# Optimization experiments

Measured on AMD Instinct MI355X. Metric: run time of the kernel, lower is better.

## Reference

```python
import jax, jax.numpy as jnp
import numpy as np

N_VALUES = 4
N_DIGITS = 7
N_CLASSES = 10
INPUT_DIM = 2048
BATCH = 32768


def setup_inputs() -> dict:
    key = jax.random.key(0)
    k1, k2, k3, k4 = jax.random.split(key, 4)
    hidden = jax.random.normal(k1, (BATCH, INPUT_DIM), dtype=jnp.float32)
    labels = jax.random.randint(k2, (BATCH, N_VALUES, N_DIGITS), 0, N_CLASSES, dtype=jnp.int64)
    H = N_VALUES * N_DIGITS  # 28 heads
    # nn.Linear default init: U(-1/sqrt(fan_in), 1/sqrt(fan_in))
    bound = 1.0 / np.sqrt(INPUT_DIM)
    W = jax.random.uniform(k3, (H, N_CLASSES, INPUT_DIM), minval=-bound, maxval=bound, dtype=jnp.float32)
    b = jax.random.uniform(k4, (H, N_CLASSES), minval=-bound, maxval=bound, dtype=jnp.float32)
    return {"hidden": hidden, "labels": labels, "W": W, "b": b}


def reference(hidden, labels, W, b):
    B = hidden.shape[0]
    # Fuse all 28 tiny GEMMs into one: [B,D] x [H,C,D] -> [B,H,C]
    logits = jnp.einsum('bd,hcd->bhc', hidden, W) + b  # [B, 28, 10]
    logits = logits.reshape(B, N_VALUES, N_DIGITS, N_CLASSES)
    # per-head cross entropy (mean over batch), summed over heads, / (n_values*n_digits)
    logp = jax.nn.log_softmax(logits, axis=-1)  # [B, V, D, C]
    nll = -jnp.take_along_axis(logp, labels[..., None], axis=-1)[..., 0]  # [B, V, D]
    loss = jnp.mean(nll, axis=0).sum() / (N_VALUES * N_DIGITS)
    return loss, logits
```

## Files before the change

kernel.cpp:

```cpp
#include <hip/hip_runtime.h>
#include <hip/hip_bf16.h>

#define BATCH   32768
#define DIM     2048
#define NHEADS  28
#define NCOLS   280
#define LOSS_SCALE (1.0f / (float)(BATCH * NHEADS))

typedef __attribute__((ext_vector_type(8))) short short8;
typedef __attribute__((ext_vector_type(4))) short s4vec;
typedef __attribute__((ext_vector_type(4))) float f32x4;

__device__ __forceinline__ short f2bf(float f) {
    union { __hip_bfloat16 h; short s; } u; u.h = __float2bfloat16(f); return u.s;
}

__global__ void mvh_swz(const float* __restrict__ W, short* __restrict__ Wswz) {
    int t = blockIdx.x * 256 + threadIdx.x;
    int lane = t & 63;
    int ks = (t >> 6) & 63;
    int nt = t >> 12;
    int n = nt * 16 + (lane & 15);
    int d = ks * 32 + (lane >> 4) * 8;
    short8 v;
    #pragma unroll
    for (int j = 0; j < 8; j++) v[j] = 0;
    if (n < NCOLS) {
        const float* src = W + (size_t)n * DIM + d;
        #pragma unroll
        for (int j = 0; j < 8; j++) v[j] = f2bf(src[j]);
    }
    *(short8*)(Wswz + (size_t)t * 8) = v;
}

#define BO(k)  (8192 + ((k) % 3) * 18432)
#define CL_PITCH 292

#define SB0() __builtin_amdgcn_sched_barrier(0)
#define BARV() do { SB0(); \
    if (wave < 2) { asm volatile("s_waitcnt vmcnt(4) lgkmcnt(0)" ::: "memory"); } \
    else          { asm volatile("s_waitcnt vmcnt(3) lgkmcnt(0)" ::: "memory"); } \
    __builtin_amdgcn_s_barrier(); SB0(); \
} while (0)
#define BAR0() do { SB0(); asm volatile("s_waitcnt vmcnt(0) lgkmcnt(0)" ::: "memory"); \
    __builtin_amdgcn_s_barrier(); SB0(); } while (0)

__global__ __launch_bounds__(512, 4)
void mvh_gemm(const float* __restrict__ hidden, const short* __restrict__ Wswz,
              const float* __restrict__ bias, float* __restrict__ logits,
              const int* __restrict__ labels, float* __restrict__ loss_out) {
    __shared__ __align__(16) char lds[63488];

    const int tid  = threadIdx.x;
    const int lane = tid & 63;
    const int wave = tid >> 6;
    const int kph   = wave >> 2;
    const int wsub  = (wave >> 1) & 1;
    const int nhalf = wave & 1;
    const int l15 = lane & 15, lhi = lane >> 4;
    const int rowbase = blockIdx.x * 64;

    const int ar  = tid >> 3;
    const int ak4 = (tid & 7) * 4;
    const float* gA1 = hidden + (size_t)(rowbase + ar) * DIM + ak4;
    const int awbyte = (ar >> 4) * 1024 + ((ar & 15) + 16 * (ak4 >> 3)) * 16 + (ak4 & 4) * 2;

    f32x4 acc0[9], acc1[9];
    #pragma unroll
    for (int n = 0; n < 9; n++) { acc0[n] = (f32x4)0.0f; acc1[n] = (f32x4)0.0f; }

    f32x4 gx, gy;

#define LOADA1(reg, t) do { reg = *(const f32x4*)(gA1 + (t) * 32); SB0(); } while (0)

#define WRITEA1(aoff, reg) do { \
    s4vec w_; \
    w_[0] = f2bf(reg[0]); w_[1] = f2bf(reg[1]); w_[2] = f2bf(reg[2]); w_[3] = f2bf(reg[3]); \
    *(s4vec*)(lds + (aoff) + awbyte) = w_; \
} while (0)

#define STAGE_B(boff, kt) do { \
    _Pragma("unroll") \
    for (int i_ = 0; i_ < 3; i_++) { \
        if (i_ < 2 || tid < 128) { \
            int g_ = (i_ < 2) ? (i_ * 512 + tid) : (1024 + tid); \
            const short* gp_ = Wswz + (size_t)((g_ >> 6) * 64 + (kt)) * 512 + (g_ & 63) * 8; \
            __builtin_amdgcn_global_load_lds((const __attribute__((address_space(1))) void*)gp_, \
                (__attribute__((address_space(3))) void*)(lds + (boff) + g_ * 16), 16, 0, 0); \
        } \
    } \
    SB0(); \
} while (0)

#define COMPUTE(aoff, boff) do { \
    short8 af0_ = *(const short8*)(lds + (aoff) + (wsub * 2 + 0) * 1024 + lane * 16); \
    short8 af1_ = *(const short8*)(lds + (aoff) + (wsub * 2 + 1) * 1024 + lane * 16); \
    _Pragma("unroll") \
    for (int n_ = 0; n_ < 9; n_++) { \
        short8 bf_ = *(const short8*)(lds + (boff) + (nhalf * 9 + n_) * 1024 + lane * 16); \
        acc0[n_] = __builtin_amdgcn_mfma_f32_16x16x32_bf16(af0_, bf_, acc0[n_], 0, 0, 0); \
        acc1[n_] = __builtin_amdgcn_mfma_f32_16x16x32_bf16(af1_, bf_, acc1[n_], 0, 0, 0); \
    } \
} while (0)

    LOADA1(gx, 0);
    STAGE_B(BO(0), 0);
    WRITEA1(0, gx);
    LOADA1(gy, 1);
    STAGE_B(BO(1), 1);
    BARV();

    #pragma unroll 1
    for (int tp = 0; tp < 32; tp++) {
        const int t = tp * 2;
        if (tp < 31) { LOADA1(gx, t + 2); STAGE_B(BO(t + 2), t + 2); }
        if (kph == 0) COMPUTE(0, BO(t));
        SB0();
        WRITEA1(4096, gy);
        if (tp < 31) { BARV(); } else { BAR0(); }
        if (tp < 31) { LOADA1(gy, t + 3); STAGE_B(BO(t + 3), t + 3); }
        if (kph == 1) COMPUTE(4096, BO(t + 1));
        SB0();
        if (tp < 31) WRITEA1(0, gx);
        if (tp < 31) { BARV(); } else { BAR0(); }
    }

#undef LOADA1
#undef WRITEA1
#undef STAGE_B
#undef COMPUTE

    float* Cl  = (float*)lds;
    float* red = (float*)(lds + 38912);
    float lsum = 0.0f;

    #pragma unroll 1
    for (int s = 0; s < 2; s++) {
        __syncthreads();
        if (kph == 1 && wsub == s) {
            #pragma unroll
            for (int nf = 0; nf < 9; nf++) {
                int c = nhalf * 144 + nf * 16 + l15;
                #pragma unroll
                for (int r = 0; r < 4; r++) {
                    Cl[(lhi * 4 + r) * CL_PITCH + c]      = acc0[nf][r];
                    Cl[(16 + lhi * 4 + r) * CL_PITCH + c] = acc1[nf][r];
                }
            }
        }
        __syncthreads();
        if (kph == 0 && wsub == s) {
            #pragma unroll
            for (int nf = 0; nf < 9; nf++) {
                int c = nhalf * 144 + nf * 16 + l15;
                #pragma unroll
                for (int r = 0; r < 4; r++) {
                    Cl[(lhi * 4 + r) * CL_PITCH + c]      += acc0[nf][r];
                    Cl[(16 + lhi * 4 + r) * CL_PITCH + c] += acc1[nf][r];
                }
            }
        }
        __syncthreads();
        #pragma unroll 1
        for (int i = tid; i < 32 * 70; i += 512) {
            int lr = i / 70, ch = i - lr * 70;
            f32x4 v  = *(const f32x4*)(Cl + lr * CL_PITCH + ch * 4);
            f32x4 bv = *(const f32x4*)(bias + ch * 4);
            *(f32x4*)(logits + (size_t)(rowbase + s * 32 + lr) * NCOLS + ch * 4) = v + bv;
        }
        #pragma unroll 1
        for (int p = tid; p < 32 * NHEADS; p += 512) {
            int lr = p / NHEADS, h = p - lr * NHEADS;
            const float* x  = Cl + lr * CL_PITCH + h * 10;
            const float* bb = bias + h * 10;
            float xv[10];
            #pragma unroll
            for (int j = 0; j < 10; j++) xv[j] = x[j] + bb[j];
            float mx = xv[0];
            #pragma unroll
            for (int j = 1; j < 10; j++) mx = fmaxf(mx, xv[j]);
            float sm = 0.0f;
            #pragma unroll
            for (int j = 0; j < 10; j++) sm += __expf(xv[j] - mx);
            int lab = labels[(size_t)(rowbase + s * 32 + lr) * NHEADS + h];
            float xl = xv[0];
            #pragma unroll
            for (int j = 1; j < 10; j++) xl = (lab == j) ? xv[j] : xl;
            lsum += mx + __logf(sm) - xl;
        }
    }

    #pragma unroll
    for (int off = 32; off > 0; off >>= 1)
        lsum += __shfl_down(lsum, off, 64);
    if (lane == 0) red[wave] = lsum;
    __syncthreads();
    if (tid == 0) {
        float t = red[0] + red[1] + red[2] + red[3]
                + red[4] + red[5] + red[6] + red[7];
        atomicAdd(loss_out, t * LOSS_SCALE);
    }
}

extern "C" void kernel_launch(void* const* d_in, const int* in_sizes, int n_in,
                              void* d_out, int out_size, void* d_ws, size_t ws_size,
                              hipStream_t stream) {
    const float* hidden = (const float*)d_in[0];
    const int* labels   = (const int*)d_in[1];
    const float* W      = (const float*)d_in[2];
    const float* bias   = (const float*)d_in[3];
    float* out = (float*)d_out;
    short* Wswz = (short*)d_ws;

    (void)hipMemsetAsync(d_out, 0, sizeof(float), stream);
    mvh_swz<<<288, 256, 0, stream>>>(W, Wswz);
    mvh_gemm<<<512, 512, 0, stream>>>(hidden, Wswz, bias, out + 1, labels, out);
}
```

Measured before the change: 104.3 us.

## Split GEMM N dimension across block pairs with 4-stage A/B pipeline

Each block now covers 64 rows and only half of the 280 output columns (140, padded to 144). Launching 1024 blocks instead of 512 raises parallelism, and each wave does 9 MFMAs per k-step instead of 18. The weight swizzle is re-laid out per half and per k-tile. The K loop now uses 4-slot A and B ring buffers, with two k-tiles issued per iteration, fewer barriers, and s_setprio around the MFMAs. The cost is that each hidden row is read from global memory twice, once by each block of the pair, though paired blocks are adjacent in launch order to share cache.

```diff
diff --git a/kernel.cpp b/kernel.cpp
--- a/kernel.cpp
+++ b/kernel.cpp
@@ -17,15 +17,19 @@
 
 __global__ void mvh_swz(const float* __restrict__ W, short* __restrict__ Wswz) {
     int t = blockIdx.x * 256 + threadIdx.x;
-    int lane = t & 63;
-    int ks = (t >> 6) & 63;
-    int nt = t >> 12;
-    int n = nt * 16 + (lane & 15);
-    int d = ks * 32 + (lane >> 4) * 8;
+    int kt = t / 1152;
+    int r  = t - kt * 1152;
+    int f  = r >> 6;
+    int l  = r & 63;
+    int nh2 = (f >= 9) ? 1 : 0;
+    int nf  = f - nh2 * 9;
+    int lc  = nf * 16 + (l & 15);
+    int n   = nh2 * 140 + lc;
+    int d   = kt * 32 + (l >> 4) * 8;
     short8 v;
     #pragma unroll
     for (int j = 0; j < 8; j++) v[j] = 0;
-    if (n < NCOLS) {
+    if (lc < 140) {
         const float* src = W + (size_t)n * DIM + d;
         #pragma unroll
         for (int j = 0; j < 8; j++) v[j] = f2bf(src[j]);
@@ -33,45 +37,45 @@
     *(short8*)(Wswz + (size_t)t * 8) = v;
 }
 
-#define BO(k)  (8192 + ((k) % 3) * 18432)
-#define CL_PITCH 292
+#define ASL(t) (((t) & 3) * 4096)
+#define BSL(t) (16384 + ((t) & 3) * 9216)
+#define CLP 148
 
 #define SB0() __builtin_amdgcn_sched_barrier(0)
-#define BARV() do { SB0(); \
-    if (wave < 2) { asm volatile("s_waitcnt vmcnt(4) lgkmcnt(0)" ::: "memory"); } \
-    else          { asm volatile("s_waitcnt vmcnt(3) lgkmcnt(0)" ::: "memory"); } \
-    __builtin_amdgcn_s_barrier(); SB0(); \
-} while (0)
-#define BAR0() do { SB0(); asm volatile("s_waitcnt vmcnt(0) lgkmcnt(0)" ::: "memory"); \
+#define BARV2() do { SB0(); asm volatile("s_waitcnt vmcnt(2) lgkmcnt(0)" ::: "memory"); \
+    __builtin_amdgcn_s_barrier(); SB0(); } while (0)
+#define BARV0() do { SB0(); asm volatile("s_waitcnt vmcnt(0) lgkmcnt(0)" ::: "memory"); \
     __builtin_amdgcn_s_barrier(); SB0(); } while (0)
 
 __global__ __launch_bounds__(512, 4)
 void mvh_gemm(const float* __restrict__ hidden, const short* __restrict__ Wswz,
               const float* __restrict__ bias, float* __restrict__ logits,
               const int* __restrict__ labels, float* __restrict__ loss_out) {
-    __shared__ __align__(16) char lds[63488];
+    __shared__ __align__(16) char lds[53248];
 
     const int tid  = threadIdx.x;
     const int lane = tid & 63;
     const int wave = tid >> 6;
-    const int kph   = wave >> 2;
-    const int wsub  = (wave >> 1) & 1;
-    const int nhalf = wave & 1;
+    const int kph  = wave >> 2;
+    const int wsub = wave & 3;
     const int l15 = lane & 15, lhi = lane >> 4;
-    const int rowbase = blockIdx.x * 64;
+    const int bid = blockIdx.x;
+    const int rowblk = ((bid >> 4) << 3) | (bid & 7);
+    const int nh2 = (bid >> 3) & 1;
+    const int rowbase = rowblk * 64;
 
     const int ar  = tid >> 3;
     const int ak4 = (tid & 7) * 4;
-    const float* gA1 = hidden + (size_t)(rowbase + ar) * DIM + ak4;
+    const float* gAbase = hidden + (size_t)(rowbase + ar) * DIM + ak4;
     const int awbyte = (ar >> 4) * 1024 + ((ar & 15) + 16 * (ak4 >> 3)) * 16 + (ak4 & 4) * 2;
 
-    f32x4 acc0[9], acc1[9];
+    f32x4 acc[9];
     #pragma unroll
-    for (int n = 0; n < 9; n++) { acc0[n] = (f32x4)0.0f; acc1[n] = (f32x4)0.0f; }
-
-    f32x4 gx, gy;
-
-#define LOADA1(reg, t) do { reg = *(const f32x4*)(gA1 + (t) * 32); SB0(); } while (0)
+    for (int n = 0; n < 9; n++) acc[n] = (f32x4)0.0f;
+
+    f32x4 ga, gb;
+
+#define LOADA1(reg, t) do { reg = *(const f32x4*)(gAbase + (size_t)(t) * 32); SB0(); } while (0)
 
 #define WRITEA1(aoff, reg) do { \
     s4vec w_; \
@@ -81,10 +85,10 @@
 
 #define STAGE_B(boff, kt) do { \
     _Pragma("unroll") \
-    for (int i_ = 0; i_ < 3; i_++) { \
-        if (i_ < 2 || tid < 128) { \
-            int g_ = (i_ < 2) ? (i_ * 512 + tid) : (1024 + tid); \
-            const short* gp_ = Wswz + (size_t)((g_ >> 6) * 64 + (kt)) * 512 + (g_ & 63) * 8; \
+    for (int i_ = 0; i_ < 2; i_++) { \
+        if (i_ == 0 || tid < 64) { \
+            int g_ = i_ * 512 + tid; \
+            const short* gp_ = Wswz + (size_t)(kt) * 9216 + (nh2 * 9 + (g_ >> 6)) * 512 + (g_ & 63) * 8; \
             __builtin_amdgcn_global_load_lds((const __attribute__((address_space(1))) void*)gp_, \
                 (__attribute__((address_space(3))) void*)(lds + (boff) + g_ * 16), 16, 0, 0); \
         } \
@@ -93,36 +97,35 @@
 } while (0)
 
 #define COMPUTE(aoff, boff) do { \
-    short8 af0_ = *(const short8*)(lds + (aoff) + (wsub * 2 + 0) * 1024 + lane * 16); \
-    short8 af1_ = *(const short8*)(lds + (aoff) + (wsub * 2 + 1) * 1024 + lane * 16); \
+    short8 af_ = *(const short8*)(lds + (aoff) + wsub * 1024 + lane * 16); \
+    __builtin_amdgcn_s_setprio(1); \
     _Pragma("unroll") \
     for (int n_ = 0; n_ < 9; n_++) { \
-        short8 bf_ = *(const short8*)(lds + (boff) + (nhalf * 9 + n_) * 1024 + lane * 16); \
-        acc0[n_] = __builtin_amdgcn_mfma_f32_16x16x32_bf16(af0_, bf_, acc0[n_], 0, 0, 0); \
-        acc1[n_] = __builtin_amdgcn_mfma_f32_16x16x32_bf16(af1_, bf_, acc1[n_], 0, 0, 0); \
+        short8 bf_ = *(const short8*)(lds + (boff) + n_ * 1024 + lane * 16); \
+        acc[n_] = __builtin_amdgcn_mfma_f32_16x16x32_bf16(af_, bf_, acc[n_], 0, 0, 0); \
     } \
+    __builtin_amdgcn_s_setprio(0); \
 } while (0)
 
-    LOADA1(gx, 0);
-    STAGE_B(BO(0), 0);
-    WRITEA1(0, gx);
-    LOADA1(gy, 1);
-    STAGE_B(BO(1), 1);
-    BARV();
+    STAGE_B(BSL(0), 0);
+    STAGE_B(BSL(1), 1);
+    LOADA1(ga, 0); LOADA1(gb, 1);
+    WRITEA1(ASL(0), ga);
+    WRITEA1(ASL(1), gb);
+    LOADA1(ga, 2); LOADA1(gb, 3);
+    BARV2();
 
     #pragma unroll 1
-    for (int tp = 0; tp < 32; tp++) {
-        const int t = tp * 2;
-        if (tp < 31) { LOADA1(gx, t + 2); STAGE_B(BO(t + 2), t + 2); }
-        if (kph == 0) COMPUTE(0, BO(t));
+    for (int i = 0; i < 32; i++) {
+        const int T = i * 2;
+        if (i < 31) { STAGE_B(BSL(T + 2), T + 2); STAGE_B(BSL(T + 3), T + 3); }
+        if (kph == 0) COMPUTE(ASL(T), BSL(T));
+        else          COMPUTE(ASL(T + 1), BSL(T + 1));
         SB0();
-        WRITEA1(4096, gy);
-        if (tp < 31) { BARV(); } else { BAR0(); }
-        if (tp < 31) { LOADA1(gy, t + 3); STAGE_B(BO(t + 3), t + 3); }
-        if (kph == 1) COMPUTE(4096, BO(t + 1));
-        SB0();
-        if (tp < 31) WRITEA1(0, gx);
-        if (tp < 31) { BARV(); } else { BAR0(); }
+        if (i < 31) { WRITEA1(ASL(T + 2), ga); WRITEA1(ASL(T + 3), gb); }
+        if (i < 30) { LOADA1(ga, T + 4); LOADA1(gb, T + 5); }
+        if (i < 30)      { BARV2(); }
+        else if (i == 30){ BARV0(); }
     }
 
 #undef LOADA1
@@ -134,60 +137,53 @@
     float* red = (float*)(lds + 38912);
     float lsum = 0.0f;
 
+    __syncthreads();
+    if (kph == 1) {
+        #pragma unroll
+        for (int nf = 0; nf < 9; nf++) {
+            int c = nf * 16 + l15;
+            #pragma unroll
+            for (int r = 0; r < 4; r++)
+                Cl[(wsub * 16 + lhi * 4 + r) * CLP + c] = acc[nf][r];
+        }
+    }
+    __syncthreads();
+    if (kph == 0) {
+        #pragma unroll
+        for (int nf = 0; nf < 9; nf++) {
+            int c = nf * 16 + l15;
+            #pragma unroll
+            for (int r = 0; r < 4; r++)
+                Cl[(wsub * 16 + lhi * 4 + r) * CLP + c] += acc[nf][r];
+        }
+    }
+    __syncthreads();
     #pragma unroll 1
-    for (int s = 0; s < 2; s++) {
-        __syncthreads();
-        if (kph == 1 && wsub == s) {
-            #pragma unroll
-            for (int nf = 0; nf < 9; nf++) {
-                int c = nhalf * 144 + nf * 16 + l15;
-                #pragma unroll
-                for (int r = 0; r < 4; r++) {
-                    Cl[(lhi * 4 + r) * CL_PITCH + c]      = acc0[nf][r];
-                    Cl[(16 + lhi * 4 + r) * CL_PITCH + c] = acc1[nf][r];
-                }
-            }
-        }
-        __syncthreads();
-        if (kph == 0 && wsub == s) {
-            #pragma unroll
-            for (int nf = 0; nf < 9; nf++) {
-                int c = nhalf * 144 + nf * 16 + l15;
-                #pragma unroll
-                for (int r = 0; r < 4; r++) {
-                    Cl[(lhi * 4 + r) * CL_PITCH + c]      += acc0[nf][r];
-                    Cl[(16 + lhi * 4 + r) * CL_PITCH + c] += acc1[nf][r];
-                }
-            }
-        }
-        __syncthreads();
-        #pragma unroll 1
-        for (int i = tid; i < 32 * 70; i += 512) {
-            int lr = i / 70, ch = i - lr * 70;
-            f32x4 v  = *(const f32x4*)(Cl + lr * CL_PITCH + ch * 4);
-            f32x4 bv = *(const f32x4*)(bias + ch * 4);
-            *(f32x4*)(logits + (size_t)(rowbase + s * 32 + lr) * NCOLS + ch * 4) = v + bv;
-        }
-        #pragma unroll 1
-        for (int p = tid; p < 32 * NHEADS; p += 512) {
-            int lr = p / NHEADS, h = p - lr * NHEADS;
-            const float* x  = Cl + lr * CL_PITCH + h * 10;
-            const float* bb = bias + h * 10;
-            float xv[10];
-            #pragma unroll
-            for (int j = 0; j < 10; j++) xv[j] = x[j] + bb[j];
-            float mx = xv[0];
-            #pragma unroll
-            for (int j = 1; j < 10; j++) mx = fmaxf(mx, xv[j]);
-            float sm = 0.0f;
-            #pragma unroll
-            for (int j = 0; j < 10; j++) sm += __expf(xv[j] - mx);
-            int lab = labels[(size_t)(rowbase + s * 32 + lr) * NHEADS + h];
-            float xl = xv[0];
-            #pragma unroll
-            for (int j = 1; j < 10; j++) xl = (lab == j) ? xv[j] : xl;
-            lsum += mx + __logf(sm) - xl;
-        }
+    for (int i = tid; i < 64 * 35; i += 512) {
+        int lr = i / 35, ch = i - lr * 35;
+        f32x4 v  = *(const f32x4*)(Cl + lr * CLP + ch * 4);
+        f32x4 bv = *(const f32x4*)(bias + nh2 * 140 + ch * 4);
+        *(f32x4*)(logits + (size_t)(rowbase + lr) * NCOLS + nh2 * 140 + ch * 4) = v + bv;
+    }
+    #pragma unroll 1
+    for (int p = tid; p < 64 * 14; p += 512) {
+        int lr = p / 14, h = p - lr * 14;
+        const float* x  = Cl + lr * CLP + h * 10;
+        const float* bb = bias + nh2 * 140 + h * 10;
+        float xv[10];
+        #pragma unroll
+        for (int j = 0; j < 10; j++) xv[j] = x[j] + bb[j];
+        float mx = xv[0];
+        #pragma unroll
+        for (int j = 1; j < 10; j++) mx = fmaxf(mx, xv[j]);
+        float sm = 0.0f;
+        #pragma unroll
+        for (int j = 0; j < 10; j++) sm += __expf(xv[j] - mx);
+        int lab = labels[(size_t)(rowbase + lr) * NHEADS + nh2 * 14 + h];
+        float xl = xv[0];
+        #pragma unroll
+        for (int j = 1; j < 10; j++) xl = (lab == j) ? xv[j] : xl;
+        lsum += mx + __logf(sm) - xl;
     }
 
     #pragma unroll
@@ -214,5 +210,5 @@
 
     (void)hipMemsetAsync(d_out, 0, sizeof(float), stream);
     mvh_swz<<<288, 256, 0, stream>>>(W, Wswz);
-    mvh_gemm<<<512, 512, 0, stream>>>(hidden, Wswz, bias, out + 1, labels, out);
-}
+    mvh_gemm<<<1024, 512, 0, stream>>>(hidden, Wswz, bias, out + 1, labels, out);
+}
```

Measured after the change: 101.1 us. -3.0%, faster.
